# Kernel tuning notes

Hardware: AMD Instinct MI355X
Metric: run time of the kernel (lower is better)

The kernel has to match this reference:

```python
import jax, jax.numpy as jnp
import numpy as np

DIM = 512
HEADS = 8
DIM_HEAD = 64
DIM_INNER = HEADS * DIM_HEAD
NULL_KV = 2
CD_ITERS = 50
CD_K = 8.0
CD_EPS = 0.1
LN_EPS = 1e-5


def setup_inputs() -> dict:
    key = jax.random.key(0)
    k0, k1, k2, k3 = jax.random.split(key, 4)
    b, n = 1, 1024
    x = jax.random.normal(k0, (b, n, DIM), dtype=jnp.float32)
    w_qkv = jax.random.normal(k1, (DIM, 3 * DIM_INNER), dtype=jnp.float32) * (DIM ** -0.5)
    w_out = jax.random.normal(k2, (DIM_INNER, DIM), dtype=jnp.float32) * (DIM_INNER ** -0.5)
    null_kv = jax.random.normal(k3, (2, HEADS, NULL_KV, DIM_HEAD), dtype=jnp.float32)
    ln_g = jnp.ones((DIM,), dtype=jnp.float32)
    ln_b = jnp.zeros((DIM,), dtype=jnp.float32)
    return {"x": x, "w_qkv": w_qkv, "w_out": w_out, "null_kv": null_kv,
            "ln_g": ln_g, "ln_b": ln_b}


def _coor_descent(s, mask, k, n_iters, eps):
    # s: (b, h, i, j); mask True = attend. eps_decay==1 upstream => eps fixed.
    mask_value = -jnp.finfo(s.dtype).max
    logk = jnp.log(jnp.asarray(k, dtype=s.dtype))
    s = jnp.where(mask, s, mask_value)

    def step(carry, _):
        a, b = carry
        sb = jnp.where(mask, (s + b) / eps, mask_value)
        a = eps * (logk - jax.nn.logsumexp(sb, axis=-1, keepdims=True))
        b = -jax.nn.relu(-s - a)
        return (a, b), None

    a0 = jnp.zeros(s.shape[:-1] + (1,), dtype=s.dtype)
    b0 = -s
    (a, b), _ = jax.lax.scan(jax.checkpoint(step), (a0, b0), None, length=n_iters)
    scores = jnp.exp((s + a + b) / eps)
    return jnp.where(mask, scores, 0.0)


def reference(x, w_qkv, w_out, null_kv, ln_g, ln_b):
    b, n, _ = x.shape
    # LayerNorm (biased variance, torch default eps)
    mu = jnp.mean(x, axis=-1, keepdims=True)
    var = jnp.var(x, axis=-1, keepdims=True)
    xn = (x - mu) / jnp.sqrt(var + LN_EPS) * ln_g + ln_b

    qkv = xn @ w_qkv                                  # (b, n, 3*dim_inner)
    q, k, v = jnp.split(qkv, 3, axis=-1)
    to_heads = lambda t: t.reshape(b, n, HEADS, DIM_HEAD).transpose(0, 2, 1, 3)
    q, k, v = to_heads(q), to_heads(k), to_heads(v)   # (b, h, n, d)

    nk = jnp.broadcast_to(null_kv[0], (b, HEADS, NULL_KV, DIM_HEAD))
    nv = jnp.broadcast_to(null_kv[1], (b, HEADS, NULL_KV, DIM_HEAD))
    k = jnp.concatenate([nk, k], axis=-2)             # (b, h, n+nkv, d)
    v = jnp.concatenate([nv, v], axis=-2)

    q = q * (DIM_HEAD ** -0.5)
    sim = jnp.einsum('bhid,bhjd->bhij', q, k)         # (b, h, i, j)
    i, j = sim.shape[-2:]
    causal = jnp.triu(jnp.ones((i, j), dtype=bool), j - i + 1)
    mask = ~causal                                    # True = attend (null kv always visible)

    attn = _coor_descent(sim, mask, CD_K, CD_ITERS, CD_EPS)
    out = jnp.einsum('bhij,bhjd->bhid', attn, v)
    out = out.transpose(0, 2, 1, 3).reshape(b, n, DIM_INNER)
    return out @ w_out
```

## Files before the change

kernel.cpp:

```cpp
#include <hip/hip_runtime.h>
#include <math.h>

#define NHEAD 8
#define SROW 1088
#define PBF  2176
#define VSTR 1056
#define LOGK 2.0794415416798357f

typedef __bf16 bf16x8 __attribute__((ext_vector_type(8)));
typedef __bf16 bf16x4 __attribute__((ext_vector_type(4)));
typedef float  f32x4  __attribute__((ext_vector_type(4)));

__device__ __forceinline__ void split2(float v, __bf16& hi, __bf16& lo) {
    hi = (__bf16)v; lo = (__bf16)(v - (float)hi);
}

__device__ __forceinline__ float dpp_sum64(float x) {
    int v;
    v = __builtin_amdgcn_update_dpp(0, __float_as_int(x), 0x111, 0xf, 0xf, true); x += __int_as_float(v);
    v = __builtin_amdgcn_update_dpp(0, __float_as_int(x), 0x112, 0xf, 0xf, true); x += __int_as_float(v);
    v = __builtin_amdgcn_update_dpp(0, __float_as_int(x), 0x114, 0xf, 0xf, true); x += __int_as_float(v);
    v = __builtin_amdgcn_update_dpp(0, __float_as_int(x), 0x118, 0xf, 0xf, true); x += __int_as_float(v);
    v = __builtin_amdgcn_update_dpp(0, __float_as_int(x), 0x142, 0xa, 0xf, true); x += __int_as_float(v);
    v = __builtin_amdgcn_update_dpp(0, __float_as_int(x), 0x143, 0xc, 0xf, true); x += __int_as_float(v);
    return __int_as_float(__builtin_amdgcn_readlane(__float_as_int(x), 63));
}
__device__ __forceinline__ float dpp_max64(float x) {
    int v;
    v = __builtin_amdgcn_update_dpp(__float_as_int(x), __float_as_int(x), 0x111, 0xf, 0xf, false); x = fmaxf(x, __int_as_float(v));
    v = __builtin_amdgcn_update_dpp(__float_as_int(x), __float_as_int(x), 0x112, 0xf, 0xf, false); x = fmaxf(x, __int_as_float(v));
    v = __builtin_amdgcn_update_dpp(__float_as_int(x), __float_as_int(x), 0x114, 0xf, 0xf, false); x = fmaxf(x, __int_as_float(v));
    v = __builtin_amdgcn_update_dpp(__float_as_int(x), __float_as_int(x), 0x118, 0xf, 0xf, false); x = fmaxf(x, __int_as_float(v));
    v = __builtin_amdgcn_update_dpp(__float_as_int(x), __float_as_int(x), 0x142, 0xa, 0xf, false); x = fmaxf(x, __int_as_float(v));
    v = __builtin_amdgcn_update_dpp(__float_as_int(x), __float_as_int(x), 0x143, 0xc, 0xf, false); x = fmaxf(x, __int_as_float(v));
    return __int_as_float(__builtin_amdgcn_readlane(__float_as_int(x), 63));
}

__global__ __launch_bounds__(256) void prep_kernel(const float* __restrict__ x,
                                                   const float* __restrict__ g,
                                                   const float* __restrict__ bb,
                                                   const float* __restrict__ w_qkv,
                                                   const float* __restrict__ w_out,
                                                   const float* __restrict__ nkv,
                                                   __bf16* __restrict__ xnh,
                                                   __bf16* __restrict__ xnl,
                                                   __bf16* __restrict__ wqh,
                                                   __bf16* __restrict__ wql,
                                                   __bf16* __restrict__ wo,
                                                   __bf16* __restrict__ kh,
                                                   __bf16* __restrict__ kl,
                                                   __bf16* __restrict__ vT) {
    __shared__ float T[64][65];
    __shared__ float sm[2][4];
    int b = blockIdx.x, tid = threadIdx.x;

    if (b < 512) {
        int half = tid >> 7, t = tid & 127;
        int row = (b << 1) + half;
        float4 v = ((const float4*)(x + (size_t)row * 512))[t];
        float s  = v.x + v.y + v.z + v.w;
        float ss = fmaf(v.x, v.x, fmaf(v.y, v.y, fmaf(v.z, v.z, v.w * v.w)));
#pragma unroll
        for (int off = 32; off; off >>= 1) {
            s  += __shfl_down(s, off);
            ss += __shfl_down(ss, off);
        }
        int wih = (tid >> 6) & 1;
        if ((tid & 63) == 0) { sm[half][wih * 2] = s; sm[half][wih * 2 + 1] = ss; }
        __syncthreads();
        s = sm[half][0] + sm[half][2]; ss = sm[half][1] + sm[half][3];
        float mu   = s * (1.f / 512);
        float var  = ss * (1.f / 512) - mu * mu;
        float rstd = 1.f / sqrtf(var + 1e-5f);
        float4 gv = ((const float4*)g)[t];
        float4 bv = ((const float4*)bb)[t];
        float o[4];
        o[0] = (v.x - mu) * rstd * gv.x + bv.x;
        o[1] = (v.y - mu) * rstd * gv.y + bv.y;
        o[2] = (v.z - mu) * rstd * gv.z + bv.z;
        o[3] = (v.w - mu) * rstd * gv.w + bv.w;
        bf16x4 h4, l4;
#pragma unroll
        for (int e = 0; e < 4; ++e) { __bf16 hi, lo; split2(o[e], hi, lo); h4[e] = hi; l4[e] = lo; }
        *(bf16x4*)(xnh + (size_t)row * 512 + t * 4) = h4;
        *(bf16x4*)(xnl + (size_t)row * 512 + t * 4) = l4;
    } else if (b < 704) {
        int b2 = b - 512;
        int k0 = (b2 & 7) * 64, n0 = (b2 >> 3) * 64;
        int r = tid >> 2, c0 = (tid & 3) << 4;
#pragma unroll
        for (int u = 0; u < 4; ++u) {
            float4 w = *(const float4*)(w_qkv + (size_t)(k0 + r) * 1536 + n0 + c0 + 4 * u);
            T[r][c0 + 4 * u + 0] = w.x; T[r][c0 + 4 * u + 1] = w.y;
            T[r][c0 + 4 * u + 2] = w.z; T[r][c0 + 4 * u + 3] = w.w;
        }
        __syncthreads();
        int nr = tid >> 2, kc0 = (tid & 3) << 4;
#pragma unroll
        for (int u = 0; u < 4; ++u) {
            bf16x4 h4, l4;
#pragma unroll
            for (int e = 0; e < 4; ++e) {
                __bf16 hi, lo; split2(T[kc0 + 4 * u + e][nr], hi, lo);
                h4[e] = hi; l4[e] = lo;
            }
            *(bf16x4*)(wqh + (size_t)(n0 + nr) * 512 + k0 + kc0 + 4 * u) = h4;
            *(bf16x4*)(wql + (size_t)(n0 + nr) * 512 + k0 + kc0 + 4 * u) = l4;
        }
    } else if (b < 768) {
        int b2 = b - 704;
        int k0 = (b2 & 7) * 64, n0 = (b2 >> 3) * 64;
        int r = tid >> 2, c0 = (tid & 3) << 4;
#pragma unroll
        for (int u = 0; u < 4; ++u) {
            float4 w = *(const float4*)(w_out + (size_t)(k0 + r) * 512 + n0 + c0 + 4 * u);
            T[r][c0 + 4 * u + 0] = w.x; T[r][c0 + 4 * u + 1] = w.y;
            T[r][c0 + 4 * u + 2] = w.z; T[r][c0 + 4 * u + 3] = w.w;
        }
        __syncthreads();
        int nr = tid >> 2, kc0 = (tid & 3) << 4;
#pragma unroll
        for (int u = 0; u < 4; ++u) {
            bf16x4 h4;
#pragma unroll
            for (int e = 0; e < 4; ++e) h4[e] = (__bf16)T[kc0 + 4 * u + e][nr];
            *(bf16x4*)(wo + (size_t)(n0 + nr) * 512 + k0 + kc0 + 4 * u) = h4;
        }
    } else {
        int t2 = (b - 768) * 256 + tid;
        int d = t2 & 63, p = (t2 >> 6) & 1, h = t2 >> 7;
        float kvf = nkv[((0 * NHEAD + h) * 2 + p) * 64 + d];
        __bf16 hi, lo; split2(kvf, hi, lo);
        kh[((size_t)h * SROW + p) * 64 + d] = hi;
        kl[((size_t)h * SROW + p) * 64 + d] = lo;
        float vf = nkv[((NHEAD + h) * 2 + p) * 64 + d];
        vT[((size_t)(h * 64) + d) * VSTR + p] = (__bf16)vf;
        int base = t2 * 15;
#pragma unroll
        for (int e = 0; e < 15; ++e) {
            int z = base + e;
            int jj = 1026 + (z % 30);
            int hd = z / 30;
            vT[(size_t)hd * VSTR + jj] = (__bf16)0.f;
        }
    }
}

__global__ __launch_bounds__(256, 4) void qkv_mfma(const __bf16* __restrict__ xh,
                                                   const __bf16* __restrict__ xl,
                                                   const __bf16* __restrict__ bh,
                                                   const __bf16* __restrict__ bl,
                                                   __bf16* __restrict__ qh,
                                                   __bf16* __restrict__ ql,
                                                   __bf16* __restrict__ kh,
                                                   __bf16* __restrict__ kl,
                                                   __bf16* __restrict__ vT) {
    int tid = threadIdx.x, l = tid & 63, w = tid >> 6;
    int m0 = blockIdx.x * 32, n0 = blockIdx.y * 64;
    int ms = (w & 1) << 4, nh2 = (w >> 1) << 5;
    int arow = m0 + ms + (l & 15);
    f32x4 acc[2] = {};
#pragma unroll 2
    for (int ks = 0; ks < 16; ++ks) {
        int koff = ((l >> 4) << 3) + (ks << 5);
        bf16x8 ah = *(const bf16x8*)(xh + (size_t)arow * 512 + koff);
        bf16x8 al = *(const bf16x8*)(xl + (size_t)arow * 512 + koff);
#pragma unroll
        for (int ct = 0; ct < 2; ++ct) {
            int ncol = n0 + nh2 + (ct << 4) + (l & 15);
            bf16x8 bhv = *(const bf16x8*)(bh + (size_t)ncol * 512 + koff);
            bf16x8 blv = *(const bf16x8*)(bl + (size_t)ncol * 512 + koff);
            acc[ct] = __builtin_amdgcn_mfma_f32_16x16x32_bf16(ah, bhv, acc[ct], 0, 0, 0);
            acc[ct] = __builtin_amdgcn_mfma_f32_16x16x32_bf16(al, bhv, acc[ct], 0, 0, 0);
            acc[ct] = __builtin_amdgcn_mfma_f32_16x16x32_bf16(ah, blv, acc[ct], 0, 0, 0);
        }
    }
#pragma unroll
    for (int ct = 0; ct < 2; ++ct) {
        int c = n0 + nh2 + (ct << 4) + (l & 15);
#pragma unroll
        for (int r = 0; r < 4; ++r) {
            int m = m0 + ms + ((l >> 4) << 2) + r;
            float val = acc[ct][r];
            if (c < 512) {
                int h = c >> 6, d = c & 63;
                __bf16 hi, lo; split2(val * 1.25f, hi, lo);
                qh[(((size_t)(h << 10)) + m) * 64 + d] = hi;
                ql[(((size_t)(h << 10)) + m) * 64 + d] = lo;
            } else if (c < 1024) {
                int c2 = c - 512, h = c2 >> 6, d = c2 & 63;
                __bf16 hi, lo; split2(val, hi, lo);
                kh[((size_t)h * SROW + 2 + m) * 64 + d] = hi;
                kl[((size_t)h * SROW + 2 + m) * 64 + d] = lo;
            } else {
                int c2 = c - 1024, h = c2 >> 6, d = c2 & 63;
                vT[((size_t)(h * 64) + d) * VSTR + 2 + m] = (__bf16)val;
            }
        }
    }
}

__global__ __launch_bounds__(256, 4) void qk_mfma(const __bf16* __restrict__ qh,
                                                  const __bf16* __restrict__ ql,
                                                  const __bf16* __restrict__ kh,
                                                  const __bf16* __restrict__ kl,
                                                  float* __restrict__ s) {
    int b = blockIdx.x, h = blockIdx.y;
    int ti = (int)((-3.0f + sqrtf(9.0f + 8.0f * (float)b)) * 0.5f);
    while ((ti + 1) * (ti + 4) / 2 <= b) ++ti;
    while (ti * (ti + 3) / 2 > b) --ti;
    int tj = b - ti * (ti + 3) / 2;
    int i0 = ti << 6, j0 = tj << 6;

    int tid = threadIdx.x, l = tid & 63, w = tid >> 6;
    int arow = i0 + (w << 4) + (l & 15);
    const __bf16* qhb = qh + ((size_t)(h << 10) + arow) * 64;
    const __bf16* qlb = ql + ((size_t)(h << 10) + arow) * 64;
    f32x4 acc[4] = {};
#pragma unroll
    for (int ks = 0; ks < 2; ++ks) {
        int koff = ((l >> 4) << 3) + (ks << 5);
        bf16x8 ah = *(const bf16x8*)(qhb + koff);
        bf16x8 al = *(const bf16x8*)(qlb + koff);
#pragma unroll
        for (int ct = 0; ct < 4; ++ct) {
            int j = j0 + (ct << 4) + (l & 15);
            bf16x8 bhv = *(const bf16x8*)(kh + ((size_t)h * SROW + j) * 64 + koff);
            bf16x8 blv = *(const bf16x8*)(kl + ((size_t)h * SROW + j) * 64 + koff);
            acc[ct] = __builtin_amdgcn_mfma_f32_16x16x32_bf16(ah, bhv, acc[ct], 0, 0, 0);
            acc[ct] = __builtin_amdgcn_mfma_f32_16x16x32_bf16(al, bhv, acc[ct], 0, 0, 0);
            acc[ct] = __builtin_amdgcn_mfma_f32_16x16x32_bf16(ah, blv, acc[ct], 0, 0, 0);
        }
    }
#pragma unroll
    for (int ct = 0; ct < 4; ++ct) {
        int j = j0 + (ct << 4) + (l & 15);
#pragma unroll
        for (int r = 0; r < 4; ++r) {
            int i = i0 + (w << 4) + ((l >> 4) << 2) + r;
            s[((size_t)(h << 10) + i) * SROW + j] = acc[ct][r];
        }
    }
}

__global__ __launch_bounds__(128, 8) void cd_kernel(float* __restrict__ s) {
    int lane = threadIdx.x & 63;
    int p = (blockIdx.x << 1) + (threadIdx.x >> 6);
    int h = p >> 9, ip = p & 511;
    int iA = 1023 - ip, iB = ip;
    int nvA = iA + 3, nvB = iB + 3;
    float* rA = s + ((size_t)(h << 10) + iA) * SROW;
    float* rB = s + ((size_t)(h << 10) + iB) * SROW;
    int jb = lane << 2;

    float4 EA[5], EB[3];
#pragma unroll
    for (int t = 0; t < 5; ++t) {
        if (jb + (t << 8) < SROW) EA[t] = *(const float4*)(rA + jb + (t << 8));
        else { EA[t].x = EA[t].y = EA[t].z = EA[t].w = -INFINITY; }
    }
#pragma unroll
    for (int t = 0; t < 3; ++t) EB[t] = *(const float4*)(rB + jb + (t << 8));

    float mA = -INFINITY, mB = -INFINITY;
#pragma unroll
    for (int t = 0; t < 5; ++t) {
        float* sp = (float*)&EA[t];
#pragma unroll
        for (int c = 0; c < 4; ++c) {
            int j = jb + c + (t << 8);
            float v = (j < nvA) ? sp[c] : -INFINITY;
            sp[c] = v; mA = fmaxf(mA, v);
        }
    }
#pragma unroll
    for (int t = 0; t < 3; ++t) {
        float* sp = (float*)&EB[t];
#pragma unroll
        for (int c = 0; c < 4; ++c) {
            int j = jb + c + (t << 8);
            float v = (j < nvB) ? sp[c] : -INFINITY;
            sp[c] = v; mB = fmaxf(mB, v);
        }
    }
    mA = dpp_max64(mA); mB = dpp_max64(mB);

#pragma unroll
    for (int t = 0; t < 5; ++t) {
        float* sp = (float*)&EA[t];
#pragma unroll
        for (int c = 0; c < 4; ++c) sp[c] = __expf(sp[c] - mA);
    }
#pragma unroll
    for (int t = 0; t < 3; ++t) {
        float* sp = (float*)&EB[t];
#pragma unroll
        for (int c = 0; c < 4; ++c) sp[c] = __expf(sp[c] - mB);
    }

    float gA = LOGK - __logf((float)nvA) + mA;
    float gB = LOGK - __logf((float)nvB) + mB;
    bool dA = false, dB = false;
#pragma unroll 1
    for (int it = 1; it < 50; ++it) {
        if (!dA) {
            float eg = __expf(fminf(gA, 80.f));
            float a0 = 0.f, a1 = 0.f, a2 = 0.f, a3 = 0.f;
#pragma unroll
            for (int t = 0; t < 5; ++t) {
                float* ep = (float*)&EA[t];
                a0 += ep[0] * fminf(1.f, ep[0] * eg);
                a1 += ep[1] * fminf(1.f, ep[1] * eg);
                a2 += ep[2] * fminf(1.f, ep[2] * eg);
                a3 += ep[3] * fminf(1.f, ep[3] * eg);
            }
            float sum = dpp_sum64((a0 + a1) + (a2 + a3));
            float g2 = LOGK - __logf(sum);
            dA = (__float_as_int(g2) == __float_as_int(gA));
            gA = g2;
        }
        if (!dB) {
            float eg = __expf(fminf(gB, 80.f));
            float b0 = 0.f, b1 = 0.f, b2 = 0.f, b3 = 0.f;
#pragma unroll
            for (int t = 0; t < 3; ++t) {
                float* ep = (float*)&EB[t];
                b0 += ep[0] * fminf(1.f, ep[0] * eg);
                b1 += ep[1] * fminf(1.f, ep[1] * eg);
                b2 += ep[2] * fminf(1.f, ep[2] * eg);
                b3 += ep[3] * fminf(1.f, ep[3] * eg);
            }
            float sum = dpp_sum64((b0 + b1) + (b2 + b3));
            float g2 = LOGK - __logf(sum);
            dB = (__float_as_int(g2) == __float_as_int(gB));
            gB = g2;
        }
        if (dA && dB) break;
    }

    float egA = __expf(fminf(gA, 80.f));
    float egB = __expf(fminf(gB, 80.f));
    __bf16* pA = (__bf16*)rA;
    __bf16* pB = (__bf16*)rB;
#pragma unroll
    for (int t = 0; t < 5; ++t) {
        if (jb + (t << 8) < SROW) {
            bf16x4 pv;
            float* ep = (float*)&EA[t];
#pragma unroll
            for (int c = 0; c < 4; ++c) {
                float wv = ep[c] * egA;
                pv[c] = (__bf16)(wv * fminf(1.f, wv));
            }
            *(bf16x4*)(pA + jb + (t << 8)) = pv;
        }
    }
#pragma unroll
    for (int t = 0; t < 3; ++t) {
        bf16x4 pv;
        float* ep = (float*)&EB[t];
#pragma unroll
        for (int c = 0; c < 4; ++c) {
            float wv = ep[c] * egB;
            pv[c] = (__bf16)(wv * fminf(1.f, wv));
        }
        *(bf16x4*)(pB + jb + (t << 8)) = pv;
    }
    bf16x4 z4 = {};
#pragma unroll
    for (int t = 3; t < 5; ++t) {
        if (jb + (t << 8) < SROW) *(bf16x4*)(pB + jb + (t << 8)) = z4;
    }
}

__global__ __launch_bounds__(256, 4) void pv_mfma(const float* __restrict__ s,
                                                  const __bf16* __restrict__ vT,
                                                  __bf16* __restrict__ ao) {
    int i0 = blockIdx.x << 4, h = blockIdx.y;
    int tid = threadIdx.x, l = tid & 63, w = tid >> 6;
    const __bf16* pbase = (const __bf16*)s;
    int arow = i0 + (l & 15);
    int dcol = (w << 4) + (l & 15);
    const __bf16* pr = pbase + ((size_t)(h << 10) + arow) * PBF;
    const __bf16* vr = vT + ((size_t)(h << 6) + dcol) * VSTR;
    f32x4 acc0 = {}, acc1 = {};
    int kb = (l >> 4) << 3;
#pragma unroll 4
    for (int ks = 0; ks < 32; ks += 2) {
        bf16x8 a0 = *(const bf16x8*)(pr + kb + (ks << 5));
        bf16x8 b0 = *(const bf16x8*)(vr + kb + (ks << 5));
        bf16x8 a1 = *(const bf16x8*)(pr + kb + ((ks + 1) << 5));
        bf16x8 b1 = *(const bf16x8*)(vr + kb + ((ks + 1) << 5));
        acc0 = __builtin_amdgcn_mfma_f32_16x16x32_bf16(a0, b0, acc0, 0, 0, 0);
        acc1 = __builtin_amdgcn_mfma_f32_16x16x32_bf16(a1, b1, acc1, 0, 0, 0);
    }
    {
        bf16x8 a0 = *(const bf16x8*)(pr + kb + (32 << 5));
        bf16x8 b0 = *(const bf16x8*)(vr + kb + (32 << 5));
        acc0 = __builtin_amdgcn_mfma_f32_16x16x32_bf16(a0, b0, acc0, 0, 0, 0);
    }
#pragma unroll
    for (int r = 0; r < 4; ++r) {
        int i = i0 + ((l >> 4) << 2) + r;
        ao[(size_t)i * 512 + (h << 6) + dcol] = (__bf16)(acc0[r] + acc1[r]);
    }
}

__global__ __launch_bounds__(256, 4) void out_mfma(const __bf16* __restrict__ ao,
                                                   const __bf16* __restrict__ wo,
                                                   float* __restrict__ out) {
    int m0 = blockIdx.x << 4, bn = blockIdx.y;
    int tid = threadIdx.x, l = tid & 63, w = tid >> 6;
    int arow = m0 + (l & 15);
    int ncol = (bn << 6) + (w << 4) + (l & 15);
    const __bf16* ar = ao + (size_t)arow * 512;
    const __bf16* br = wo + (size_t)ncol * 512;
    f32x4 acc0 = {}, acc1 = {};
    int kb = (l >> 4) << 3;
#pragma unroll 4
    for (int ks = 0; ks < 16; ks += 2) {
        bf16x8 a0 = *(const bf16x8*)(ar + kb + (ks << 5));
        bf16x8 b0 = *(const bf16x8*)(br + kb + (ks << 5));
        bf16x8 a1 = *(const bf16x8*)(ar + kb + ((ks + 1) << 5));
        bf16x8 b1 = *(const bf16x8*)(br + kb + ((ks + 1) << 5));
        acc0 = __builtin_amdgcn_mfma_f32_16x16x32_bf16(a0, b0, acc0, 0, 0, 0);
        acc1 = __builtin_amdgcn_mfma_f32_16x16x32_bf16(a1, b1, acc1, 0, 0, 0);
    }
#pragma unroll
    for (int r = 0; r < 4; ++r) {
        int m = m0 + ((l >> 4) << 2) + r;
        out[(size_t)m * 512 + ncol] = acc0[r] + acc1[r];
    }
}

extern "C" void kernel_launch(void* const* d_in, const int* in_sizes, int n_in,
                              void* d_out, int out_size, void* d_ws, size_t ws_size,
                              hipStream_t stream) {
    const float* x      = (const float*)d_in[0];
    const float* w_qkv  = (const float*)d_in[1];
    const float* w_out  = (const float*)d_in[2];
    const float* nullkv = (const float*)d_in[3];
    const float* ln_g   = (const float*)d_in[4];
    const float* ln_b   = (const float*)d_in[5];
    float* ws = (float*)d_ws;
    float* out = (float*)d_out;

    float* base = ws;
    __bf16* xnh = (__bf16*)(base);              base += 262144;
    __bf16* xnl = (__bf16*)(base);              base += 262144;
    __bf16* wqh = (__bf16*)(base);              base += 393216;
    __bf16* wql = (__bf16*)(base);              base += 393216;
    __bf16* qh  = (__bf16*)(base);              base += 262144;
    __bf16* ql  = (__bf16*)(base);              base += 262144;
    __bf16* kh  = (__bf16*)(base);              base += 278528;
    __bf16* kl  = (__bf16*)(base);              base += 278528;
    __bf16* vT  = (__bf16*)(base);              base += 270336;
    __bf16* wo  = (__bf16*)(base);              base += 131072;
    __bf16* ao  = (__bf16*)(base);              base += 262144;
    float*  s   = base;

    hipLaunchKernelGGL(prep_kernel, dim3(772),    dim3(256), 0, stream,
                       x, ln_g, ln_b, w_qkv, w_out, nullkv,
                       xnh, xnl, wqh, wql, wo, kh, kl, vT);
    hipLaunchKernelGGL(qkv_mfma,   dim3(32, 24),  dim3(256), 0, stream, xnh, xnl, wqh, wql, qh, ql, kh, kl, vT);
    hipLaunchKernelGGL(qk_mfma,    dim3(152, 8),  dim3(256), 0, stream, qh, ql, kh, kl, s);
    hipLaunchKernelGGL(cd_kernel,  dim3(2048),    dim3(128), 0, stream, s);
    hipLaunchKernelGGL(pv_mfma,    dim3(64, 8),   dim3(256), 0, stream, s, vT, ao);
    hipLaunchKernelGGL(out_mfma,   dim3(64, 8),   dim3(256), 0, stream, ao, wo, out);
}
```

Measured before the change: 171.8 us.

## Fuse QK^T score computation into coordinate-descent kernel via LDS staging

```diff
diff --git a/kernel.cpp b/kernel.cpp
--- a/kernel.cpp
+++ b/kernel.cpp
@@ -3,7 +3,7 @@
 
 #define NHEAD 8
 #define SROW 1088
-#define PBF  2176
+#define PSTR 1088
 #define VSTR 1056
 #define LOGK 2.0794415416798357f
 
@@ -200,68 +200,58 @@
     }
 }
 
-__global__ __launch_bounds__(256, 4) void qk_mfma(const __bf16* __restrict__ qh,
-                                                  const __bf16* __restrict__ ql,
-                                                  const __bf16* __restrict__ kh,
-                                                  const __bf16* __restrict__ kl,
-                                                  float* __restrict__ s) {
-    int b = blockIdx.x, h = blockIdx.y;
-    int ti = (int)((-3.0f + sqrtf(9.0f + 8.0f * (float)b)) * 0.5f);
-    while ((ti + 1) * (ti + 4) / 2 <= b) ++ti;
-    while (ti * (ti + 3) / 2 > b) --ti;
-    int tj = b - ti * (ti + 3) / 2;
-    int i0 = ti << 6, j0 = tj << 6;
-
+__global__ __launch_bounds__(512, 4) void qkcd_kernel(const __bf16* __restrict__ qh,
+                                                      const __bf16* __restrict__ ql,
+                                                      const __bf16* __restrict__ kh,
+                                                      const __bf16* __restrict__ kl,
+                                                      __bf16* __restrict__ pbuf) {
+    __shared__ float s_lds[1040 * 17];
     int tid = threadIdx.x, l = tid & 63, w = tid >> 6;
-    int arow = i0 + (w << 4) + (l & 15);
-    const __bf16* qhb = qh + ((size_t)(h << 10) + arow) * 64;
-    const __bf16* qlb = ql + ((size_t)(h << 10) + arow) * 64;
-    f32x4 acc[4] = {};
-#pragma unroll
-    for (int ks = 0; ks < 2; ++ks) {
-        int koff = ((l >> 4) << 3) + (ks << 5);
-        bf16x8 ah = *(const bf16x8*)(qhb + koff);
-        bf16x8 al = *(const bf16x8*)(qlb + koff);
-#pragma unroll
-        for (int ct = 0; ct < 4; ++ct) {
-            int j = j0 + (ct << 4) + (l & 15);
-            bf16x8 bhv = *(const bf16x8*)(kh + ((size_t)h * SROW + j) * 64 + koff);
-            bf16x8 blv = *(const bf16x8*)(kl + ((size_t)h * SROW + j) * 64 + koff);
-            acc[ct] = __builtin_amdgcn_mfma_f32_16x16x32_bf16(ah, bhv, acc[ct], 0, 0, 0);
-            acc[ct] = __builtin_amdgcn_mfma_f32_16x16x32_bf16(al, bhv, acc[ct], 0, 0, 0);
-            acc[ct] = __builtin_amdgcn_mfma_f32_16x16x32_bf16(ah, blv, acc[ct], 0, 0, 0);
-        }
-    }
-#pragma unroll
-    for (int ct = 0; ct < 4; ++ct) {
-        int j = j0 + (ct << 4) + (l & 15);
-#pragma unroll
-        for (int r = 0; r < 4; ++r) {
-            int i = i0 + (w << 4) + ((l >> 4) << 2) + r;
-            s[((size_t)(h << 10) + i) * SROW + j] = acc[ct][r];
-        }
-    }
-}
-
-__global__ __launch_bounds__(128, 8) void cd_kernel(float* __restrict__ s) {
-    int lane = threadIdx.x & 63;
-    int p = (blockIdx.x << 1) + (threadIdx.x >> 6);
-    int h = p >> 9, ip = p & 511;
+    int ip0 = blockIdx.x << 3, h = blockIdx.y;
+    int ext = 1026 - ip0;
+    int T = (ext + 15) >> 4;
+
+    int c16 = l & 15;
+    int kgrp = (l >> 4) << 3;
+    int row16 = (c16 < 8) ? (1016 - ip0 + c16) : (ip0 + c16 - 8);
+    const __bf16* qrb = qh + ((size_t)(h << 10) + row16) * 64 + kgrp;
+    const __bf16* qrl = ql + ((size_t)(h << 10) + row16) * 64 + kgrp;
+    bf16x8 qB0 = *(const bf16x8*)(qrb);
+    bf16x8 qB1 = *(const bf16x8*)(qrb + 32);
+    bf16x8 qL0 = *(const bf16x8*)(qrl);
+    bf16x8 qL1 = *(const bf16x8*)(qrl + 32);
+
+    const __bf16* khb = kh + ((size_t)h * SROW) * 64;
+    const __bf16* klb = kl + ((size_t)h * SROW) * 64;
+    for (int jt = w; jt < T; jt += 8) {
+        int jg = (jt << 4) + c16;
+        const __bf16* ka = khb + (size_t)jg * 64 + kgrp;
+        const __bf16* kb = klb + (size_t)jg * 64 + kgrp;
+        f32x4 acc = {};
+        bf16x8 ah0 = *(const bf16x8*)(ka);
+        bf16x8 al0 = *(const bf16x8*)(kb);
+        bf16x8 ah1 = *(const bf16x8*)(ka + 32);
+        bf16x8 al1 = *(const bf16x8*)(kb + 32);
+        acc = __builtin_amdgcn_mfma_f32_16x16x32_bf16(ah0, qB0, acc, 0, 0, 0);
+        acc = __builtin_amdgcn_mfma_f32_16x16x32_bf16(al0, qB0, acc, 0, 0, 0);
+        acc = __builtin_amdgcn_mfma_f32_16x16x32_bf16(ah0, qL0, acc, 0, 0, 0);
+        acc = __builtin_amdgcn_mfma_f32_16x16x32_bf16(ah1, qB1, acc, 0, 0, 0);
+        acc = __builtin_amdgcn_mfma_f32_16x16x32_bf16(al1, qB1, acc, 0, 0, 0);
+        acc = __builtin_amdgcn_mfma_f32_16x16x32_bf16(ah1, qL1, acc, 0, 0, 0);
+        int jb0 = (jt << 4) + ((l >> 4) << 2);
+#pragma unroll
+        for (int r = 0; r < 4; ++r)
+            s_lds[(jb0 + r) * 17 + c16] = acc[r];
+    }
+    __syncthreads();
+
+    int ip = ip0 + w;
     int iA = 1023 - ip, iB = ip;
     int nvA = iA + 3, nvB = iB + 3;
-    float* rA = s + ((size_t)(h << 10) + iA) * SROW;
-    float* rB = s + ((size_t)(h << 10) + iB) * SROW;
-    int jb = lane << 2;
+    int colA = 7 - w, colB = 8 + w;
+    int jb = l << 2;
 
     float4 EA[5], EB[3];
-#pragma unroll
-    for (int t = 0; t < 5; ++t) {
-        if (jb + (t << 8) < SROW) EA[t] = *(const float4*)(rA + jb + (t << 8));
-        else { EA[t].x = EA[t].y = EA[t].z = EA[t].w = -INFINITY; }
-    }
-#pragma unroll
-    for (int t = 0; t < 3; ++t) EB[t] = *(const float4*)(rB + jb + (t << 8));
-
     float mA = -INFINITY, mB = -INFINITY;
 #pragma unroll
     for (int t = 0; t < 5; ++t) {
@@ -269,7 +259,7 @@
 #pragma unroll
         for (int c = 0; c < 4; ++c) {
             int j = jb + c + (t << 8);
-            float v = (j < nvA) ? sp[c] : -INFINITY;
+            float v = (j < nvA) ? s_lds[j * 17 + colA] : -INFINITY;
             sp[c] = v; mA = fmaxf(mA, v);
         }
     }
@@ -279,7 +269,7 @@
 #pragma unroll
         for (int c = 0; c < 4; ++c) {
             int j = jb + c + (t << 8);
-            float v = (j < nvB) ? sp[c] : -INFINITY;
+            float v = (j < nvB) ? s_lds[j * 17 + colB] : -INFINITY;
             sp[c] = v; mB = fmaxf(mB, v);
         }
     }
@@ -340,11 +330,11 @@
 
     float egA = __expf(fminf(gA, 80.f));
     float egB = __expf(fminf(gB, 80.f));
-    __bf16* pA = (__bf16*)rA;
-    __bf16* pB = (__bf16*)rB;
+    __bf16* pA = pbuf + ((size_t)(h << 10) + iA) * PSTR;
+    __bf16* pB = pbuf + ((size_t)(h << 10) + iB) * PSTR;
 #pragma unroll
     for (int t = 0; t < 5; ++t) {
-        if (jb + (t << 8) < SROW) {
+        if (jb + (t << 8) < PSTR) {
             bf16x4 pv;
             float* ep = (float*)&EA[t];
 #pragma unroll
@@ -369,19 +359,18 @@
     bf16x4 z4 = {};
 #pragma unroll
     for (int t = 3; t < 5; ++t) {
-        if (jb + (t << 8) < SROW) *(bf16x4*)(pB + jb + (t << 8)) = z4;
-    }
-}
-
-__global__ __launch_bounds__(256, 4) void pv_mfma(const float* __restrict__ s,
+        if (jb + (t << 8) < PSTR) *(bf16x4*)(pB + jb + (t << 8)) = z4;
+    }
+}
+
+__global__ __launch_bounds__(256, 4) void pv_mfma(const __bf16* __restrict__ pbuf,
                                                   const __bf16* __restrict__ vT,
                                                   __bf16* __restrict__ ao) {
     int i0 = blockIdx.x << 4, h = blockIdx.y;
     int tid = threadIdx.x, l = tid & 63, w = tid >> 6;
-    const __bf16* pbase = (const __bf16*)s;
     int arow = i0 + (l & 15);
     int dcol = (w << 4) + (l & 15);
-    const __bf16* pr = pbase + ((size_t)(h << 10) + arow) * PBF;
+    const __bf16* pr = pbuf + ((size_t)(h << 10) + arow) * PSTR;
     const __bf16* vr = vT + ((size_t)(h << 6) + dcol) * VSTR;
     f32x4 acc0 = {}, acc1 = {};
     int kb = (l >> 4) << 3;
@@ -457,14 +446,13 @@
     __bf16* vT  = (__bf16*)(base);              base += 270336;
     __bf16* wo  = (__bf16*)(base);              base += 131072;
     __bf16* ao  = (__bf16*)(base);              base += 262144;
-    float*  s   = base;
+    __bf16* pbuf = (__bf16*)(base);
 
     hipLaunchKernelGGL(prep_kernel, dim3(772),    dim3(256), 0, stream,
                        x, ln_g, ln_b, w_qkv, w_out, nullkv,
                        xnh, xnl, wqh, wql, wo, kh, kl, vT);
     hipLaunchKernelGGL(qkv_mfma,   dim3(32, 24),  dim3(256), 0, stream, xnh, xnl, wqh, wql, qh, ql, kh, kl, vT);
-    hipLaunchKernelGGL(qk_mfma,    dim3(152, 8),  dim3(256), 0, stream, qh, ql, kh, kl, s);
-    hipLaunchKernelGGL(cd_kernel,  dim3(2048),    dim3(128), 0, stream, s);
-    hipLaunchKernelGGL(pv_mfma,    dim3(64, 8),   dim3(256), 0, stream, s, vT, ao);
+    hipLaunchKernelGGL(qkcd_kernel, dim3(64, 8),  dim3(512), 0, stream, qh, ql, kh, kl, pbuf);
+    hipLaunchKernelGGL(pv_mfma,    dim3(64, 8),   dim3(256), 0, stream, pbuf, vT, ao);
     hipLaunchKernelGGL(out_mfma,   dim3(64, 8),   dim3(256), 0, stream, ao, wo, out);
 }
```

After: 172.7 us. About the same (+0.5%).
